# Kernel tuning notes

Hardware: AMD Instinct MI355X
Metric: run time of the kernel (lower is better)

## Reference

```python
import jax, jax.numpy as jnp
import numpy as np

DIM = 1024
NUM_HEADS = 16
HEAD_DIM = DIM // NUM_HEADS
WINDOW = 16
B, S = 2, 8192
MAX_POS = 8192


def setup_inputs() -> dict:
    key = jax.random.key(0)
    ks = jax.random.split(key, 6)
    x = jax.random.normal(ks[0], (B, S, DIM), dtype=jnp.float32)
    # rope angle table [max_pos, head_dim//2]
    rope_freqs = jax.random.uniform(ks[1], (MAX_POS, HEAD_DIM // 2), dtype=jnp.float32)
    scale = 1.0 / np.sqrt(DIM)
    wq = jax.random.normal(ks[2], (DIM, DIM), dtype=jnp.float32) * scale
    wk = jax.random.normal(ks[3], (DIM, DIM), dtype=jnp.float32) * scale
    wv = jax.random.normal(ks[4], (DIM, DIM), dtype=jnp.float32) * scale
    wo = jax.random.normal(ks[5], (DIM, DIM), dtype=jnp.float32) * scale
    return {"x": x, "rope_freqs": rope_freqs, "wq": wq, "wk": wk, "wv": wv, "wo": wo}


def _apply_rope(t, cos, sin):
    # t: [N, W, H, hd]; cos/sin: [1, W, 1, hd//2] (split-half rotation)
    t1, t2 = jnp.split(t, 2, axis=-1)
    return jnp.concatenate([t1 * cos - t2 * sin, t1 * sin + t2 * cos], axis=-1)


def reference(x, rope_freqs, wq, wk, wv, wo):
    Bx, Sx, D = x.shape
    W, H, hd = WINDOW, NUM_HEADS, HEAD_DIM
    n_windows = Sx // W  # S chosen divisible by W (pad = 0 path)
    xw = x.reshape(Bx * n_windows, W, D)
    q = (xw @ wq.T).reshape(Bx * n_windows, W, H, hd)
    k = (xw @ wk.T).reshape(Bx * n_windows, W, H, hd)
    v = (xw @ wv.T).reshape(Bx * n_windows, W, H, hd)
    # position_ids=None path: positions are arange(W) in every window
    freqs = rope_freqs[jnp.arange(W)]                 # [W, hd//2]
    cos = jnp.cos(freqs)[None, :, None, :]
    sin = jnp.sin(freqs)[None, :, None, :]
    q = _apply_rope(q, cos, sin)
    k = _apply_rope(k, cos, sin)
    # non-causal flash attention within each window
    scores = jnp.einsum('nqhd,nkhd->nhqk', q, k) / jnp.sqrt(jnp.float32(hd))
    probs = jax.nn.softmax(scores, axis=-1)
    attn = jnp.einsum('nhqk,nkhd->nqhd', probs, v)    # [B*nw, W, H, hd]
    attn = attn.reshape(Bx, Sx, H * hd)
    return attn @ wo.T
```

## Files before the change

### kernel.cpp

```cpp
#include <hip/hip_runtime.h>
#include <hip/hip_bf16.h>
#include <stdint.h>

typedef short bf16x8 __attribute__((ext_vector_type(8)));
typedef short bf16x4 __attribute__((ext_vector_type(4)));
typedef float f32x4  __attribute__((ext_vector_type(4)));

__device__ __forceinline__ float b2f(short s) {
  union { float f; uint32_t u; } x;
  x.u = ((uint32_t)(uint16_t)s) << 16;
  return x.f;
}
__device__ __forceinline__ short f2b(float f) {
  union { float f; uint32_t u; } x;
  x.f = f;
  uint32_t r = x.u + 0x7fff + ((x.u >> 16) & 1);
  return (short)(r >> 16);
}

__device__ __forceinline__ void gload_lds16(const void* g, void* l) {
  __builtin_amdgcn_global_load_lds(
      (const __attribute__((address_space(1))) void*)g,
      (__attribute__((address_space(3))) void*)l, 16, 0, 0);
}

__global__ __launch_bounds__(256)
void prep(const float* __restrict__ x, const float* __restrict__ rope,
          const float* __restrict__ wq, const float* __restrict__ wk,
          const float* __restrict__ wv, const float* __restrict__ wo,
          short* __restrict__ Xb, short* __restrict__ Wqkv, short* __restrict__ Wob,
          float* __restrict__ costab, float* __restrict__ sintab)
{
  const int64_t XN4 = 16777216 / 4;
  const int64_t WN4 = 1048576 / 4;
  const int64_t total = XN4 + 4 * WN4 + 512;
  for (int64_t i = (int64_t)blockIdx.x * blockDim.x + threadIdx.x; i < total;
       i += (int64_t)gridDim.x * blockDim.x) {
    if (i < XN4) {
      f32x4 v = ((const f32x4*)x)[i];
      bf16x4 o;
#pragma unroll
      for (int j = 0; j < 4; ++j) o[j] = f2b(v[j]);
      ((bf16x4*)Xb)[i] = o;
    } else if (i < XN4 + 3 * WN4) {
      int64_t j = i - XN4;
      const float* src = (j < WN4) ? wq : ((j < 2 * WN4) ? wk : wv);
      int64_t jj = j & (WN4 - 1);
      f32x4 v = ((const f32x4*)src)[jj];
      bf16x4 o;
#pragma unroll
      for (int q = 0; q < 4; ++q) o[q] = f2b(v[q]);
      ((bf16x4*)Wqkv)[j] = o;
    } else if (i < XN4 + 4 * WN4) {
      int64_t j = i - XN4 - 3 * WN4;
      f32x4 v = ((const f32x4*)wo)[j];
      bf16x4 o;
#pragma unroll
      for (int q = 0; q < 4; ++q) o[q] = f2b(v[q]);
      ((bf16x4*)Wob)[j] = o;
    } else {
      int64_t j = i - XN4 - 4 * WN4;
      int pos = (int)(j >> 5), f = (int)(j & 31);
      float a = rope[pos * 32 + f];
      costab[j] = cosf(a);
      sintab[j] = sinf(a);
    }
  }
}

__device__ __forceinline__ void storeC(short* C, size_t idx, float v) { C[idx] = f2b(v); }
__device__ __forceinline__ void storeC(float* C, size_t idx, float v) { C[idx] = v; }

template <typename OutT>
__global__ __launch_bounds__(256)
void gemm_bt(const short* __restrict__ A, const short* __restrict__ Bw,
             OutT* __restrict__ C, int M, int N, int K)
{
  __shared__ short As[128 * 32];
  __shared__ short Bs[128 * 32];
  const int t = threadIdx.x;
  const int lane = t & 63;
  const int wid = t >> 6;
  const int wm = wid >> 1, wn = wid & 1;
  const int ntn = N >> 7;
  const int m0 = (blockIdx.x / ntn) << 7;
  const int n0 = (blockIdx.x % ntn) << 7;

  const int lr = lane & 15;
  const int lk = (lane >> 4) << 3;

  f32x4 acc[4][4];
#pragma unroll
  for (int m = 0; m < 4; ++m)
#pragma unroll
    for (int n = 0; n < 4; ++n) acc[m][n] = (f32x4){0.f, 0.f, 0.f, 0.f};

  const int c0 = wid * 2, c1 = wid * 2 + 1;
  const int e0 = (c0 * 64 + lane) * 8, e1 = (c1 * 64 + lane) * 8;
  const int r0 = e0 >> 5, cc0 = e0 & 31;
  const int r1 = e1 >> 5, cc1 = e1 & 31;

  for (int k0 = 0; k0 < K; k0 += 32) {
    gload_lds16(A + (size_t)(m0 + r0) * K + k0 + cc0, (char*)As + c0 * 1024);
    gload_lds16(A + (size_t)(m0 + r1) * K + k0 + cc1, (char*)As + c1 * 1024);
    gload_lds16(Bw + (size_t)(n0 + r0) * K + k0 + cc0, (char*)Bs + c0 * 1024);
    gload_lds16(Bw + (size_t)(n0 + r1) * K + k0 + cc1, (char*)Bs + c1 * 1024);
    asm volatile("s_waitcnt vmcnt(0)" ::: "memory");
    __syncthreads();

    bf16x8 af[4], bfr[4];
#pragma unroll
    for (int m = 0; m < 4; ++m)
      af[m] = *(const bf16x8*)&As[(wm * 64 + m * 16 + lr) * 32 + lk];
#pragma unroll
    for (int n = 0; n < 4; ++n)
      bfr[n] = *(const bf16x8*)&Bs[(wn * 64 + n * 16 + lr) * 32 + lk];
#pragma unroll
    for (int m = 0; m < 4; ++m)
#pragma unroll
      for (int n = 0; n < 4; ++n)
        acc[m][n] = __builtin_amdgcn_mfma_f32_16x16x32_bf16(af[m], bfr[n], acc[m][n], 0, 0, 0);
    __syncthreads();
  }

  const int orow = m0 + wm * 64 + ((lane >> 4) << 2);
  const int ocol = n0 + wn * 64 + lr;
#pragma unroll
  for (int m = 0; m < 4; ++m)
#pragma unroll
    for (int n = 0; n < 4; ++n) {
      f32x4 v = acc[m][n];
#pragma unroll
      for (int i = 0; i < 4; ++i)
        storeC(C, (size_t)(orow + m * 16 + i) * N + (ocol + n * 16), v[i]);
    }
}

__global__ __launch_bounds__(256)
void attn_win(const short* __restrict__ QKV,
              const float* __restrict__ costab, const float* __restrict__ sintab,
              short* __restrict__ Attn)
{
  __shared__ float Plds[4][16][17];
  __shared__ short Vlds[4][16][64];
  const int t = threadIdx.x, lane = t & 63, wid = t >> 6;
  const int pair = blockIdx.x * 4 + wid;
  const int win = pair >> 4, h = pair & 15;
  const int lr = lane & 15;
  const int lk = (lane >> 4) << 3;

  const size_t rowb = (size_t)(win * 16 + lr) * 3072;
  const short* qp = QKV + rowb + h * 64;
  const short* kp = qp + 1024;

  bf16x8 q0 = *(const bf16x8*)(qp + lk);
  bf16x8 q1 = *(const bf16x8*)(qp + 32 + lk);
  bf16x8 k0 = *(const bf16x8*)(kp + lk);
  bf16x8 k1 = *(const bf16x8*)(kp + 32 + lk);

#pragma unroll
  for (int j = 0; j < 2; ++j) {
    int e = (j * 64 + lane) * 8;
    int vr = e >> 6, vc = e & 63;
    *(bf16x8*)&Vlds[wid][vr][vc] =
        *(const bf16x8*)(QKV + (size_t)(win * 16 + vr) * 3072 + 2048 + h * 64 + vc);
  }

  bf16x8 a0, a1, b0, b1;
#pragma unroll
  for (int j = 0; j < 8; ++j) {
    int f = lk + j;
    float c = costab[lr * 32 + f], s = sintab[lr * 32 + f];
    float x1 = b2f(q0[j]), x2 = b2f(q1[j]);
    a0[j] = f2b(x1 * c - x2 * s);
    a1[j] = f2b(x1 * s + x2 * c);
    float y1 = b2f(k0[j]), y2 = b2f(k1[j]);
    b0[j] = f2b(y1 * c - y2 * s);
    b1[j] = f2b(y1 * s + y2 * c);
  }

  f32x4 sc = (f32x4){0.f, 0.f, 0.f, 0.f};
  sc = __builtin_amdgcn_mfma_f32_16x16x32_bf16(a0, b0, sc, 0, 0, 0);
  sc = __builtin_amdgcn_mfma_f32_16x16x32_bf16(a1, b1, sc, 0, 0, 0);

  float p[4];
#pragma unroll
  for (int i = 0; i < 4; ++i) {
    float v = sc[i] * 0.125f;
    float m = v;
#pragma unroll
    for (int msk = 1; msk < 16; msk <<= 1) m = fmaxf(m, __shfl_xor(m, msk));
    float e = __expf(v - m);
    float s = e;
#pragma unroll
    for (int msk = 1; msk < 16; msk <<= 1) s += __shfl_xor(s, msk);
    p[i] = e / s;
  }
#pragma unroll
  for (int i = 0; i < 4; ++i)
    Plds[wid][((lane >> 4) << 2) + i][lr] = p[i];

  __syncthreads();

  const int r = lr, dblk = lane >> 4;
  float a[16];
#pragma unroll
  for (int j = 0; j < 16; ++j) a[j] = 0.f;
#pragma unroll
  for (int k = 0; k < 16; ++k) {
    float pk = Plds[wid][r][k];
    bf16x8 v0 = *(const bf16x8*)&Vlds[wid][k][dblk * 16];
    bf16x8 v1 = *(const bf16x8*)&Vlds[wid][k][dblk * 16 + 8];
#pragma unroll
    for (int j = 0; j < 8; ++j) {
      a[j]     += pk * b2f(v0[j]);
      a[8 + j] += pk * b2f(v1[j]);
    }
  }
  bf16x8 o0, o1;
#pragma unroll
  for (int j = 0; j < 8; ++j) { o0[j] = f2b(a[j]); o1[j] = f2b(a[8 + j]); }
  short* op = Attn + (size_t)(win * 16 + r) * 1024 + h * 64 + dblk * 16;
  *(bf16x8*)op = o0;
  *(bf16x8*)(op + 8) = o1;
}

extern "C" void kernel_launch(void* const* d_in, const int* in_sizes, int n_in,
                              void* d_out, int out_size, void* d_ws, size_t ws_size,
                              hipStream_t stream)
{
  const float* x  = (const float*)d_in[0];
  const float* rf = (const float*)d_in[1];
  const float* wq = (const float*)d_in[2];
  const float* wk = (const float*)d_in[3];
  const float* wv = (const float*)d_in[4];
  const float* wo = (const float*)d_in[5];
  float* out = (float*)d_out;

  char* w = (char*)d_ws;
  short* Xb     = (short*)(w);
  short* Wqkv   = (short*)(w + 33554432);
  short* Wob    = (short*)(w + 39845888);
  short* QKV    = (short*)(w + 41943040);
  short* Attn   = (short*)(w + 142606336);
  float* costab = (float*)(w + 176160768);
  float* sintab = (float*)(w + 176162816);

  prep<<<2048, 256, 0, stream>>>(x, rf, wq, wk, wv, wo, Xb, Wqkv, Wob, costab, sintab);
  gemm_bt<short><<<3072, 256, 0, stream>>>(Xb, Wqkv, QKV, 16384, 3072, 1024);
  attn_win<<<4096, 256, 0, stream>>>(QKV, costab, sintab, Attn);
  gemm_bt<float><<<1024, 256, 0, stream>>>(Attn, Wob, out, 16384, 1024, 1024);
}
```

Measured before the change: 366.5 us.

## Rewrite GEMMs with triple-buffered LDS pipeline, swizzled tiles and larger blocks

Replaces the single-buffered 128x128xK32 GEMM with a 512-thread 128x256 tile kernel using K=64 steps and a three-stage LDS ring. Each step prefetches two stages ahead via global_load_lds, so loads overlap the MFMAs. It also adds XOR-swizzled LDS addressing to avoid bank conflicts, workgroup index remapping for cache locality, and vectorized 4-wide output stores by swapping the MFMA operands. It uses 144KB of LDS per block, which limits occupancy to one block per CU. It also assumes the dimensions divide the tile sizes.

```diff
diff --git a/kernel.cpp b/kernel.cpp
--- a/kernel.cpp
+++ b/kernel.cpp
@@ -68,72 +68,119 @@
   }
 }
 
-__device__ __forceinline__ void storeC(short* C, size_t idx, float v) { C[idx] = f2b(v); }
-__device__ __forceinline__ void storeC(float* C, size_t idx, float v) { C[idx] = v; }
+__device__ __forceinline__ void store4(short* C, size_t idx, f32x4 v) {
+  bf16x4 o;
+#pragma unroll
+  for (int j = 0; j < 4; ++j) o[j] = f2b(v[j]);
+  *(bf16x4*)(C + idx) = o;
+}
+__device__ __forceinline__ void store4(float* C, size_t idx, f32x4 v) {
+  *(f32x4*)(C + idx) = v;
+}
 
 template <typename OutT>
-__global__ __launch_bounds__(256)
-void gemm_bt(const short* __restrict__ A, const short* __restrict__ Bw,
-             OutT* __restrict__ C, int M, int N, int K)
+__global__ __launch_bounds__(512, 2)
+void gemm_bt2(const short* __restrict__ A, const short* __restrict__ Bw,
+              OutT* __restrict__ C, int M, int N, int K, int nmt)
 {
-  __shared__ short As[128 * 32];
-  __shared__ short Bs[128 * 32];
+  __shared__ __align__(16) char lds[147456];
   const int t = threadIdx.x;
   const int lane = t & 63;
   const int wid = t >> 6;
-  const int wm = wid >> 1, wn = wid & 1;
-  const int ntn = N >> 7;
-  const int m0 = (blockIdx.x / ntn) << 7;
-  const int n0 = (blockIdx.x % ntn) << 7;
+  const int wm = wid >> 2;
+  const int wn = wid & 3;
+
+  int nwg = gridDim.x;
+  int bid = blockIdx.x;
+  int swz = ((nwg & 7) == 0) ? ((bid & 7) * (nwg >> 3) + (bid >> 3)) : bid;
+  const int mt = swz % nmt;
+  const int nt = swz / nmt;
+  const int m0 = mt << 7;
+  const int n0 = nt << 8;
+
+  const int T = K >> 6;
+
+  const int r_a  = lane >> 3;
+  const int csrc = lane & 7;
+
+  auto stageA = [&](int kt, int buf) {
+    char* base = lds + buf * 49152;
+#pragma unroll
+    for (int j = 0; j < 2; ++j) {
+      int chunk = j * 8 + wid;
+      int r = chunk * 8 + r_a;
+      int sl = csrc ^ (r & 7);
+      gload_lds16(A + (size_t)(m0 + r) * K + (kt << 6) + (sl << 3),
+                  base + chunk * 1024);
+    }
+  };
+  auto stageB = [&](int kt, int buf) {
+    char* base = lds + buf * 49152 + 16384;
+#pragma unroll
+    for (int j = 0; j < 4; ++j) {
+      int chunk = j * 8 + wid;
+      int r = chunk * 8 + r_a;
+      int sl = csrc ^ (r & 7);
+      gload_lds16(Bw + (size_t)(n0 + r) * K + (kt << 6) + (sl << 3),
+                  base + chunk * 1024);
+    }
+  };
+
+  f32x4 acc[4][4];
+#pragma unroll
+  for (int m = 0; m < 4; ++m)
+#pragma unroll
+    for (int n = 0; n < 4; ++n) acc[m][n] = (f32x4){0.f, 0.f, 0.f, 0.f};
 
   const int lr = lane & 15;
-  const int lk = (lane >> 4) << 3;
-
-  f32x4 acc[4][4];
-#pragma unroll
-  for (int m = 0; m < 4; ++m)
-#pragma unroll
-    for (int n = 0; n < 4; ++n) acc[m][n] = (f32x4){0.f, 0.f, 0.f, 0.f};
-
-  const int c0 = wid * 2, c1 = wid * 2 + 1;
-  const int e0 = (c0 * 64 + lane) * 8, e1 = (c1 * 64 + lane) * 8;
-  const int r0 = e0 >> 5, cc0 = e0 & 31;
-  const int r1 = e1 >> 5, cc1 = e1 & 31;
-
-  for (int k0 = 0; k0 < K; k0 += 32) {
-    gload_lds16(A + (size_t)(m0 + r0) * K + k0 + cc0, (char*)As + c0 * 1024);
-    gload_lds16(A + (size_t)(m0 + r1) * K + k0 + cc1, (char*)As + c1 * 1024);
-    gload_lds16(Bw + (size_t)(n0 + r0) * K + k0 + cc0, (char*)Bs + c0 * 1024);
-    gload_lds16(Bw + (size_t)(n0 + r1) * K + k0 + cc1, (char*)Bs + c1 * 1024);
-    asm volatile("s_waitcnt vmcnt(0)" ::: "memory");
-    __syncthreads();
-
-    bf16x8 af[4], bfr[4];
-#pragma unroll
-    for (int m = 0; m < 4; ++m)
-      af[m] = *(const bf16x8*)&As[(wm * 64 + m * 16 + lr) * 32 + lk];
-#pragma unroll
-    for (int n = 0; n < 4; ++n)
-      bfr[n] = *(const bf16x8*)&Bs[(wn * 64 + n * 16 + lr) * 32 + lk];
-#pragma unroll
-    for (int m = 0; m < 4; ++m)
-#pragma unroll
-      for (int n = 0; n < 4; ++n)
-        acc[m][n] = __builtin_amdgcn_mfma_f32_16x16x32_bf16(af[m], bfr[n], acc[m][n], 0, 0, 0);
-    __syncthreads();
-  }
-
-  const int orow = m0 + wm * 64 + ((lane >> 4) << 2);
-  const int ocol = n0 + wn * 64 + lr;
-#pragma unroll
-  for (int m = 0; m < 4; ++m)
-#pragma unroll
-    for (int n = 0; n < 4; ++n) {
-      f32x4 v = acc[m][n];
-#pragma unroll
-      for (int i = 0; i < 4; ++i)
-        storeC(C, (size_t)(orow + m * 16 + i) * N + (ocol + n * 16), v[i]);
-    }
+  const int ls = lane >> 4;
+  const int axor = lr & 7;
+
+  stageA(0, 0); stageB(0, 0);
+  if (T > 1) { stageA(1, 1); stageB(1, 1); }
+
+  for (int kt = 0; kt < T; ++kt) {
+    if (kt + 1 < T) asm volatile("s_waitcnt vmcnt(6)" ::: "memory");
+    else            asm volatile("s_waitcnt vmcnt(0)" ::: "memory");
+    __builtin_amdgcn_s_barrier();
+    __builtin_amdgcn_sched_barrier(0);
+
+    const int buf = kt % 3;
+    if (kt + 2 < T) { const int nb = (kt + 2) % 3; stageA(kt + 2, nb); stageB(kt + 2, nb); }
+
+    const char* ab = lds + buf * 49152;
+    const char* bb = ab + 16384;
+    bf16x8 af[2][4], bfr[2][4];
+#pragma unroll
+    for (int kk = 0; kk < 2; ++kk) {
+      const int u = (((kk << 2) + ls) ^ axor) << 4;
+#pragma unroll
+      for (int m4 = 0; m4 < 4; ++m4)
+        af[kk][m4] = *(const bf16x8*)(ab + (wm * 64 + m4 * 16 + lr) * 128 + u);
+#pragma unroll
+      for (int n4 = 0; n4 < 4; ++n4)
+        bfr[kk][n4] = *(const bf16x8*)(bb + (wn * 64 + n4 * 16 + lr) * 128 + u);
+    }
+
+    __builtin_amdgcn_s_setprio(1);
+#pragma unroll
+    for (int kk = 0; kk < 2; ++kk)
+#pragma unroll
+      for (int m4 = 0; m4 < 4; ++m4)
+#pragma unroll
+        for (int n4 = 0; n4 < 4; ++n4)
+          acc[m4][n4] = __builtin_amdgcn_mfma_f32_16x16x32_bf16(
+              bfr[kk][n4], af[kk][m4], acc[m4][n4], 0, 0, 0);
+    __builtin_amdgcn_s_setprio(0);
+  }
+
+  const int orow = m0 + wm * 64 + lr;
+  const int ocol = n0 + wn * 64 + ls * 4;
+#pragma unroll
+  for (int m4 = 0; m4 < 4; ++m4)
+#pragma unroll
+    for (int n4 = 0; n4 < 4; ++n4)
+      store4(C, (size_t)(orow + m4 * 16) * N + (ocol + n4 * 16), acc[m4][n4]);
 }
 
 __global__ __launch_bounds__(256)
@@ -247,7 +294,7 @@
   float* sintab = (float*)(w + 176162816);
 
   prep<<<2048, 256, 0, stream>>>(x, rf, wq, wk, wv, wo, Xb, Wqkv, Wob, costab, sintab);
-  gemm_bt<short><<<3072, 256, 0, stream>>>(Xb, Wqkv, QKV, 16384, 3072, 1024);
+  gemm_bt2<short><<<1536, 512, 0, stream>>>(Xb, Wqkv, QKV, 16384, 3072, 1024, 128);
   attn_win<<<4096, 256, 0, stream>>>(QKV, costab, sintab, Attn);
-  gemm_bt<float><<<1024, 256, 0, stream>>>(Attn, Wob, out, 16384, 1024, 1024);
-}
+  gemm_bt2<float><<<512, 512, 0, stream>>>(Attn, Wob, out, 16384, 1024, 1024, 128);
+}
```

Measured after the change: 353.8 us. 1.04x faster.
